# Optimization experiments

Measured on AMD Instinct MI355X. Metric: run time of the kernel, lower is better.

The kernel has to match this reference:

```python
import jax, jax.numpy as jnp
import numpy as np

F = 128   # num_features
H = 128   # hidden sizes
U = 128   # u_size == out_size
N = 50000
E = 600000
B = 64
L = 4     # hops + 1 layers


def _scatter_mean(vals, idx, num_segments):
    s = jax.ops.segment_sum(vals, idx, num_segments=num_segments)
    cnt = jax.ops.segment_sum(jnp.ones((vals.shape[0],), vals.dtype), idx,
                              num_segments=num_segments)
    return s / jnp.maximum(cnt, 1.0)[:, None]


def setup_inputs() -> dict:
    key = jax.random.key(0)
    ks = jax.random.split(key, 20)
    x = jax.random.normal(ks[0], (N, F), jnp.float32)
    edge_index = jax.random.randint(ks[1], (2, E), 0, N, jnp.int64)
    u = jax.random.normal(ks[2], (B, U), jnp.float32)
    batch = jnp.sort(jax.random.randint(ks[3], (N,), 0, B, jnp.int64))
    sc = 0.05
    # stacked per-layer params (all layer dims identical since u_size==out_size)
    params = {
        'n1w1': jax.random.normal(ks[4], (L, F, H), jnp.float32) * sc,
        'n1b1': jnp.zeros((L, H), jnp.float32),
        'n1w2': jax.random.normal(ks[5], (L, H, H), jnp.float32) * sc,
        'n1b2': jnp.zeros((L, H), jnp.float32),
        'n2w1': jax.random.normal(ks[6], (L, F + H + U, H), jnp.float32) * sc,
        'n2b1': jnp.zeros((L, H), jnp.float32),
        'n2w2': jax.random.normal(ks[7], (L, H, F), jnp.float32) * sc,
        'n2b2': jnp.zeros((L, F), jnp.float32),
        'gw1': jax.random.normal(ks[8], (L, F + U, H), jnp.float32) * sc,
        'gb1': jnp.zeros((L, H), jnp.float32),
        'gw2': jax.random.normal(ks[9], (L, H, U), jnp.float32) * sc,
        'gb2': jnp.zeros((L, U), jnp.float32),
    }
    return dict(x=x, edge_index=edge_index, u=u, batch=batch, **params)


def reference(x, edge_index, u, batch,
              n1w1, n1b1, n1w2, n1b2, n2w1, n2b1, n2w2, n2b2,
              gw1, gb1, gw2, gb2):
    row, col = edge_index[0], edge_index[1]
    for l in range(L):
        # NodeModel
        m = jax.nn.relu(x[row] @ n1w1[l] + n1b1[l]) @ n1w2[l] + n1b2[l]  # [E,H]
        agg = _scatter_mean(m, col, N)                                    # [N,H]
        h = jnp.concatenate([x, agg, u[batch]], axis=1)                   # [N,F+H+U]
        x = jax.nn.relu(h @ n2w1[l] + n2b1[l]) @ n2w2[l] + n2b2[l]        # [N,F]
        # GlobalModel (uses updated x)
        g = jnp.concatenate([u, _scatter_mean(x, batch, B)], axis=1)      # [B,F+U]
        u = jax.nn.relu(g @ gw1[l] + gb1[l]) @ gw2[l] + gb2[l]            # [B,U]
    return (x, u)
```

## Files before the change

kernel.cpp:

```cpp
#include <hip/hip_runtime.h>

typedef __bf16 bf16;
typedef bf16 bf16x8 __attribute__((ext_vector_type(8)));
typedef bf16 bf16x4 __attribute__((ext_vector_type(4)));
typedef bf16 bf16x2 __attribute__((ext_vector_type(2)));
typedef float floatx4 __attribute__((ext_vector_type(4)));

#define MFMA __builtin_amdgcn_mfma_f32_16x16x32_bf16

__device__ __forceinline__ float bfhi_f(unsigned u) {
  const unsigned x = u << 16;
  return __builtin_bit_cast(float, x);
}
__device__ __forceinline__ float bflo_f(unsigned u) {
  const unsigned x = u & 0xffff0000u;
  return __builtin_bit_cast(float, x);
}


__global__ void hist_kernel(const int* __restrict__ ei, int* __restrict__ cnt, int E) {
  int e = blockIdx.x * blockDim.x + threadIdx.x;
  if (e < E) atomicAdd(&cnt[ei[E + e]], 1);
}

__global__ void gcnt_kernel(const int* __restrict__ batch, int* __restrict__ gcnt,
                            int N, int B) {
  const int b = threadIdx.x;
  if (b >= B) return;
  auto lb = [&](int v) {
    int lo = 0, hi = N;
    while (lo < hi) {
      const int mid = (lo + hi) >> 1;
      if (batch[mid] < v) lo = mid + 1; else hi = mid;
    }
    return lo;
  };
  gcnt[b] = lb(b + 1) - lb(b);
}

__global__ void scan1_kernel(const int* __restrict__ cnt, int* __restrict__ colptr,
                             int* __restrict__ rctr, int* __restrict__ btot, int n) {
  __shared__ int sd[256];
  const int tid = threadIdx.x;
  const int i0 = blockIdx.x * 2048 + tid * 8;
  int v[8];
  int tot = 0;
#pragma unroll
  for (int j = 0; j < 8; ++j) {
    const int i = i0 + j;
    v[j] = (i < n) ? cnt[i] : 0;
    tot += v[j];
  }
  sd[tid] = tot;
  __syncthreads();
  for (int off = 1; off < 256; off <<= 1) {
    const int t = (tid >= off) ? sd[tid - off] : 0;
    __syncthreads();
    sd[tid] += t;
    __syncthreads();
  }
  int excl = sd[tid] - tot;
#pragma unroll
  for (int j = 0; j < 8; ++j) {
    const int i = i0 + j;
    if (i < n) { colptr[i] = excl; rctr[i] = excl; }
    excl += v[j];
  }
  if (tid == 255) btot[blockIdx.x] = sd[255];
}

__global__ void scan2_kernel(int* __restrict__ colptr, int* __restrict__ rctr,
                             const int* __restrict__ btot, int n) {
  __shared__ int off_s;
  const int tid = threadIdx.x;
  if (blockIdx.x == 0) return;
  if (tid == 0) {
    int o = 0;
    for (int j = 0; j < (int)blockIdx.x; ++j) o += btot[j];
    off_s = o;
  }
  __syncthreads();
  const int off = off_s;
  const int i0 = blockIdx.x * 2048 + tid * 8;
#pragma unroll
  for (int j = 0; j < 8; ++j) {
    const int i = i0 + j;
    if (i < n) { colptr[i] += off; rctr[i] += off; }
  }
}

__global__ void place_kernel(const int* __restrict__ ei, int* __restrict__ rctr,
                             int* __restrict__ esrow, int E) {
  int e = blockIdx.x * blockDim.x + threadIdx.x;
  if (e >= E) return;
  const int r = ei[e];
  const int c = ei[E + e];
  const int p = atomicAdd(&rctr[c], 1);
  esrow[p] = r;
}

__global__ void wsplit_kernel(const float* __restrict__ src, bf16* __restrict__ dst,
                              int Ksrc, int K, int HH) {
  const int l = blockIdx.y;
  const int gid = blockIdx.x * blockDim.x + threadIdx.x;
  if (gid >= K * HH) return;
  const int h = gid / K, k = gid - h * K;
  const float v = src[(size_t)l * Ksrc * HH + (size_t)k * HH + h];
  const bf16 hi = (bf16)v;
  const bf16 lo = (bf16)(v - (float)hi);
  bf16* d = dst + (size_t)l * 2 * K * HH;
  d[(size_t)h * K + k] = hi;
  d[(size_t)K * HH + (size_t)h * K + k] = lo;
}

__global__ void xsplit_kernel(const float* __restrict__ x, bf16* __restrict__ xhi,
                              bf16* __restrict__ xlo, int n4) {
  const int i = blockIdx.x * 256 + threadIdx.x;
  if (i >= n4) return;
  const float4 v = ((const float4*)x)[i];
  bf16x4 h, l;
  const float vv[4] = {v.x, v.y, v.z, v.w};
#pragma unroll
  for (int r = 0; r < 4; ++r) {
    h[r] = (bf16)vv[r];
    l[r] = (bf16)(vv[r] - (float)h[r]);
  }
  *(bf16x4*)&xhi[(size_t)i * 4] = h;
  *(bf16x4*)&xlo[(size_t)i * 4] = l;
}

__global__ __launch_bounds__(256, 4)
void pnode_mfma(const bf16* __restrict__ xh, const bf16* __restrict__ xl,
                const bf16* __restrict__ w1t, const float* __restrict__ b1,
                const bf16* __restrict__ w2t, const float* __restrict__ b2,
                bf16* __restrict__ P, int N) {
  __shared__ __align__(16) bf16 R[2 * 64 * 136];

  const int tid = threadIdx.x;
  const int n0 = blockIdx.x * 64;
  const int wave = tid >> 6, lane = tid & 63, q = lane >> 4, lr = lane & 15;
  const int hbase = wave * 32;

  int nn[4];
#pragma unroll
  for (int nt = 0; nt < 4; ++nt) {
    int n = n0 + nt * 16 + lr;
    nn[nt] = (n > N - 1) ? (N - 1) : n;
  }

  const floatx4 zz = {0.f, 0.f, 0.f, 0.f};
  floatx4 acc[2][4];
#pragma unroll
  for (int mt = 0; mt < 2; ++mt)
#pragma unroll
    for (int nt = 0; nt < 4; ++nt) acc[mt][nt] = zz;

  {
    bf16x8 bh[2][4], bl[2][4];
#pragma unroll
    for (int nt = 0; nt < 4; ++nt) {
      const size_t off = (size_t)nn[nt] * 128 + q * 8;
      bh[0][nt] = *(const bf16x8*)(xh + off);
      bl[0][nt] = *(const bf16x8*)(xl + off);
    }
#pragma unroll
    for (int kc = 0; kc < 4; ++kc) {
      const int cur = kc & 1, nxt = cur ^ 1;
      if (kc < 3) {
#pragma unroll
        for (int nt = 0; nt < 4; ++nt) {
          const size_t off = (size_t)nn[nt] * 128 + (kc + 1) * 32 + q * 8;
          bh[nxt][nt] = *(const bf16x8*)(xh + off);
          bl[nxt][nt] = *(const bf16x8*)(xl + off);
        }
      }
      bf16x8 ah[2], al[2];
#pragma unroll
      for (int mt = 0; mt < 2; ++mt) {
        const bf16* wp = w1t + (size_t)(hbase + mt * 16 + lr) * 128 + kc * 32 + q * 8;
        ah[mt] = *(const bf16x8*)wp;
        al[mt] = *(const bf16x8*)(wp + 16384);
      }
#pragma unroll
      for (int nt = 0; nt < 4; ++nt)
#pragma unroll
        for (int mt = 0; mt < 2; ++mt) {
          acc[mt][nt] = MFMA(ah[mt], bh[cur][nt], acc[mt][nt], 0, 0, 0);
          acc[mt][nt] = MFMA(al[mt], bh[cur][nt], acc[mt][nt], 0, 0, 0);
          acc[mt][nt] = MFMA(ah[mt], bl[cur][nt], acc[mt][nt], 0, 0, 0);
        }
    }
  }

#pragma unroll
  for (int mt = 0; mt < 2; ++mt) {
    const int h0 = hbase + mt * 16 + q * 4;
    const float* bp = &b1[h0];
#pragma unroll
    for (int nt = 0; nt < 4; ++nt) {
      const int e = nt * 16 + lr;
      bf16x4 hh, ll;
#pragma unroll
      for (int r = 0; r < 4; ++r) {
        const float v = fmaxf(acc[mt][nt][r] + bp[r], 0.f);
        hh[r] = (bf16)v;
        ll[r] = (bf16)(v - (float)hh[r]);
      }
      *(bf16x4*)&R[e * 136 + h0] = hh;
      *(bf16x4*)&R[64 * 136 + e * 136 + h0] = ll;
      acc[mt][nt] = zz;
    }
  }
  __syncthreads();

#pragma unroll
  for (int ks = 0; ks < 4; ++ks) {
    bf16x8 ah[2], al[2], b2h[4], b2l[4];
#pragma unroll
    for (int mt = 0; mt < 2; ++mt) {
      const bf16* wp = w2t + (size_t)(hbase + mt * 16 + lr) * 128 + ks * 32 + q * 8;
      ah[mt] = *(const bf16x8*)wp;
      al[mt] = *(const bf16x8*)(wp + 16384);
    }
#pragma unroll
    for (int nt = 0; nt < 4; ++nt) {
      const bf16* hp = &R[(nt * 16 + lr) * 136 + ks * 32 + q * 8];
      b2h[nt] = *(const bf16x8*)hp;
      b2l[nt] = *(const bf16x8*)(hp + 64 * 136);
    }
#pragma unroll
    for (int nt = 0; nt < 4; ++nt)
#pragma unroll
      for (int mt = 0; mt < 2; ++mt) {
        acc[mt][nt] = MFMA(ah[mt], b2h[nt], acc[mt][nt], 0, 0, 0);
        acc[mt][nt] = MFMA(al[mt], b2h[nt], acc[mt][nt], 0, 0, 0);
        acc[mt][nt] = MFMA(ah[mt], b2l[nt], acc[mt][nt], 0, 0, 0);
      }
  }
  __syncthreads();

#pragma unroll
  for (int mt = 0; mt < 2; ++mt) {
    const int f0 = hbase + mt * 16 + q * 4;
    const float* bp = &b2[f0];
#pragma unroll
    for (int nt = 0; nt < 4; ++nt) {
      const int e = nt * 16 + lr;
      bf16x4 o;
#pragma unroll
      for (int r = 0; r < 4; ++r) o[r] = (bf16)(acc[mt][nt][r] + bp[r]);
      *(bf16x4*)&R[e * 136 + f0] = o;
    }
  }
  __syncthreads();
#pragma unroll
  for (int it = 0; it < 4; ++it) {
    const int idx = it * 256 + tid;
    const int row = idx >> 4;
    const int f8 = (idx & 15) * 8;
    const int n = n0 + row;
    if (n < N)
      *(bf16x8*)&P[(size_t)n * 128 + f8] = *(const bf16x8*)&R[row * 136 + f8];
  }
}

__global__ __launch_bounds__(256, 8)
void agg_csr(const bf16* __restrict__ P, const int* __restrict__ colptr,
             const int* __restrict__ esrow,
             bf16* __restrict__ aggh, bf16* __restrict__ aggl, int N, int E) {
  const int lane = threadIdx.x & 63;
  const int c = blockIdx.x * 4 + (threadIdx.x >> 6);
  if (c >= N) return;
  const int beg = colptr[c];
  const int end = (c == N - 1) ? E : colptr[c + 1];
  float s0[4] = {0.f, 0.f, 0.f, 0.f};
  float s1[4] = {0.f, 0.f, 0.f, 0.f};
  int e = beg;
  for (; e + 8 <= end; e += 8) {
    int r[8];
#pragma unroll
    for (int j = 0; j < 8; ++j) r[j] = esrow[e + j];
    unsigned v[8];
#pragma unroll
    for (int j = 0; j < 8; ++j)
      v[j] = *(const unsigned*)&P[(size_t)r[j] * 128 + lane * 2];
#pragma unroll
    for (int j = 0; j < 8; ++j) {
      s0[j & 3] += bfhi_f(v[j]);
      s1[j & 3] += bflo_f(v[j]);
    }
  }
  const int rem = end - e;
  if (rem > 0) {
    int r[8];
#pragma unroll
    for (int j = 0; j < 8; ++j) r[j] = esrow[e + (j < rem ? j : 0)];
    unsigned v[8];
#pragma unroll
    for (int j = 0; j < 8; ++j)
      v[j] = *(const unsigned*)&P[(size_t)r[j] * 128 + lane * 2];
#pragma unroll
    for (int j = 0; j < 8; ++j) {
      if (j < rem) {
        s0[j & 3] += bfhi_f(v[j]);
        s1[j & 3] += bflo_f(v[j]);
      }
    }
  }
  const int cc = end - beg;
  const float inv = 1.f / (float)(cc > 1 ? cc : 1);
  const float v0 = ((s0[0] + s0[1]) + (s0[2] + s0[3])) * inv;
  const float v1 = ((s1[0] + s1[1]) + (s1[2] + s1[3])) * inv;
  bf16x2 h, l;
  h[0] = (bf16)v0;  l[0] = (bf16)(v0 - (float)h[0]);
  h[1] = (bf16)v1;  l[1] = (bf16)(v1 - (float)h[1]);
  *(bf16x2*)&aggh[(size_t)c * 128 + lane * 2] = h;
  *(bf16x2*)&aggl[(size_t)c * 128 + lane * 2] = l;
}

__global__ __launch_bounds__(256, 4)
void node_p(bf16* xh, bf16* xl,
            const bf16* __restrict__ aggh, const bf16* __restrict__ aggl,
            const float* __restrict__ UW, const int* __restrict__ batch,
            const bf16* __restrict__ w1t, const bf16* __restrict__ w2t,
            const float* __restrict__ b2,
            const bf16* __restrict__ w1te, const float* __restrict__ b1e,
            const bf16* __restrict__ w2te, const float* __restrict__ b2e,
            bf16* __restrict__ Pout, float* __restrict__ gx,
            float* __restrict__ xout, int write_x, int has_next, int N) {
  __shared__ __align__(16) bf16 R[2 * 64 * 136];
  __shared__ int sbatch[64];

  const int tid = threadIdx.x;
  const int n0 = blockIdx.x * 64;
  const int wave = tid >> 6, lane = tid & 63, q = lane >> 4, lr = lane & 15;
  const int hbase = wave * 32;

  if (tid < 64) {
    int n = n0 + tid;
    sbatch[tid] = batch[(n > N - 1) ? (N - 1) : n];
  }

  int nn[4], ub[4];
#pragma unroll
  for (int nt = 0; nt < 4; ++nt) {
    int n = n0 + nt * 16 + lr;
    if (n > N - 1) n = N - 1;
    nn[nt] = n;
    ub[nt] = batch[n];
  }

  floatx4 acc[2][4];
#pragma unroll
  for (int mt = 0; mt < 2; ++mt)
#pragma unroll
    for (int nt = 0; nt < 4; ++nt)
      acc[mt][nt] = *(const floatx4*)&UW[(size_t)ub[nt] * 128 + hbase + mt * 16 + q * 4];

  {
    bf16x8 bh[2][4], bl[2][4];
    auto loadB = [&](int kc, int buf) {
#pragma unroll
      for (int nt = 0; nt < 4; ++nt) {
        if (kc < 4) {
          const size_t off = (size_t)nn[nt] * 128 + kc * 32 + q * 8;
          bh[buf][nt] = *(const bf16x8*)(xh + off);
          bl[buf][nt] = *(const bf16x8*)(xl + off);
        } else {
          const size_t off = (size_t)nn[nt] * 128 + (kc - 4) * 32 + q * 8;
          bh[buf][nt] = *(const bf16x8*)(aggh + off);
          bl[buf][nt] = *(const bf16x8*)(aggl + off);
        }
      }
    };
    loadB(0, 0);
#pragma unroll
    for (int kc = 0; kc < 8; ++kc) {
      const int cur = kc & 1, nxt = cur ^ 1;
      if (kc < 7) loadB(kc + 1, nxt);
      bf16x8 ah[2], al[2];
#pragma unroll
      for (int mt = 0; mt < 2; ++mt) {
        const bf16* wp = w1t + (size_t)(hbase + mt * 16 + lr) * 256 + kc * 32 + q * 8;
        ah[mt] = *(const bf16x8*)wp;
        al[mt] = *(const bf16x8*)(wp + 32768);
      }
#pragma unroll
      for (int nt = 0; nt < 4; ++nt)
#pragma unroll
        for (int mt = 0; mt < 2; ++mt) {
          acc[mt][nt] = MFMA(ah[mt], bh[cur][nt], acc[mt][nt], 0, 0, 0);
          acc[mt][nt] = MFMA(al[mt], bh[cur][nt], acc[mt][nt], 0, 0, 0);
          acc[mt][nt] = MFMA(ah[mt], bl[cur][nt], acc[mt][nt], 0, 0, 0);
        }
    }
  }

  const floatx4 zz = {0.f, 0.f, 0.f, 0.f};
#pragma unroll
  for (int mt = 0; mt < 2; ++mt) {
    const int h0 = hbase + mt * 16 + q * 4;
#pragma unroll
    for (int nt = 0; nt < 4; ++nt) {
      const int e = nt * 16 + lr;
      bf16x4 hh, ll;
#pragma unroll
      for (int r = 0; r < 4; ++r) {
        const float v = fmaxf(acc[mt][nt][r], 0.f);
        hh[r] = (bf16)v;
        ll[r] = (bf16)(v - (float)hh[r]);
      }
      *(bf16x4*)&R[e * 136 + h0] = hh;
      *(bf16x4*)&R[64 * 136 + e * 136 + h0] = ll;
      acc[mt][nt] = zz;
    }
  }
  __syncthreads();

#pragma unroll
  for (int ks = 0; ks < 4; ++ks) {
    bf16x8 ah[2], al[2], b2h[4], b2l[4];
#pragma unroll
    for (int mt = 0; mt < 2; ++mt) {
      const bf16* wp = w2t + (size_t)(hbase + mt * 16 + lr) * 128 + ks * 32 + q * 8;
      ah[mt] = *(const bf16x8*)wp;
      al[mt] = *(const bf16x8*)(wp + 16384);
    }
#pragma unroll
    for (int nt = 0; nt < 4; ++nt) {
      const bf16* hp = &R[(nt * 16 + lr) * 136 + ks * 32 + q * 8];
      b2h[nt] = *(const bf16x8*)hp;
      b2l[nt] = *(const bf16x8*)(hp + 64 * 136);
    }
#pragma unroll
    for (int nt = 0; nt < 4; ++nt)
#pragma unroll
      for (int mt = 0; mt < 2; ++mt) {
        acc[mt][nt] = MFMA(ah[mt], b2h[nt], acc[mt][nt], 0, 0, 0);
        acc[mt][nt] = MFMA(al[mt], b2h[nt], acc[mt][nt], 0, 0, 0);
        acc[mt][nt] = MFMA(ah[mt], b2l[nt], acc[mt][nt], 0, 0, 0);
      }
  }
  __syncthreads();

  float* Xt = (float*)&R[0];
#pragma unroll
  for (int mt = 0; mt < 2; ++mt) {
    const int f0 = hbase + mt * 16 + q * 4;
    const float* bp = &b2[f0];
#pragma unroll
    for (int nt = 0; nt < 4; ++nt) {
      const int e = nt * 16 + lr;
      const int n = n0 + e;
      float4 o;
      o.x = (n < N) ? acc[mt][nt][0] + bp[0] : 0.f;
      o.y = (n < N) ? acc[mt][nt][1] + bp[1] : 0.f;
      o.z = (n < N) ? acc[mt][nt][2] + bp[2] : 0.f;
      o.w = (n < N) ? acc[mt][nt][3] + bp[3] : 0.f;
      *(float4*)&Xt[e * 132 + f0] = o;
    }
  }
  __syncthreads();

  if (has_next) {
#pragma unroll
    for (int it = 0; it < 4; ++it) {
      const int idx = it * 256 + tid;
      const int row = idx >> 4;
      const int f8 = (idx & 15) * 8;
      const int n = n0 + row;
      if (n < N) {
        bf16x8 hh, ll;
#pragma unroll
        for (int j = 0; j < 8; ++j) {
          const float v = Xt[row * 132 + f8 + j];
          hh[j] = (bf16)v;
          ll[j] = (bf16)(v - (float)hh[j]);
        }
        *(bf16x8*)&xh[(size_t)n * 128 + f8] = hh;
        *(bf16x8*)&xl[(size_t)n * 128 + f8] = ll;
      }
    }
  }
  if (write_x) {
#pragma unroll
    for (int it = 0; it < 8; ++it) {
      const int idx = it * 256 + tid;
      const int row = idx >> 5;
      const int f4 = (idx & 31) * 4;
      const int n = n0 + row;
      if (n < N)
        *(float4*)&xout[(size_t)n * 128 + f4] = *(const float4*)&Xt[row * 132 + f4];
    }
  }

  {
    const int f = tid & 127;
    const int es = (tid >> 7) * 32;
    int cur = sbatch[es];
    float s = 0.f;
    for (int e = es; e < es + 32; ++e) {
      const int b = sbatch[e];
      const float v = Xt[e * 132 + f];
      if (b != cur) {
        atomicAdd(&gx[(size_t)cur * 128 + f], s);
        s = 0.f;
        cur = b;
      }
      s += v;
    }
    atomicAdd(&gx[(size_t)cur * 128 + f], s);
  }

  if (!has_next) return;

#pragma unroll
  for (int mt = 0; mt < 2; ++mt)
#pragma unroll
    for (int nt = 0; nt < 4; ++nt) acc[mt][nt] = zz;

#pragma unroll
  for (int kc = 0; kc < 4; ++kc) {
    bf16x8 ah[2], al[2], bh[4], bl[4];
#pragma unroll
    for (int mt = 0; mt < 2; ++mt) {
      const bf16* wp = w1te + (size_t)(hbase + mt * 16 + lr) * 128 + kc * 32 + q * 8;
      ah[mt] = *(const bf16x8*)wp;
      al[mt] = *(const bf16x8*)(wp + 16384);
    }
#pragma unroll
    for (int nt = 0; nt < 4; ++nt) {
      const float* xp = &Xt[(nt * 16 + lr) * 132 + kc * 32 + q * 8];
#pragma unroll
      for (int r = 0; r < 8; ++r) {
        const float v = xp[r];
        bh[nt][r] = (bf16)v;
        bl[nt][r] = (bf16)(v - (float)bh[nt][r]);
      }
    }
#pragma unroll
    for (int nt = 0; nt < 4; ++nt)
#pragma unroll
      for (int mt = 0; mt < 2; ++mt) {
        acc[mt][nt] = MFMA(ah[mt], bh[nt], acc[mt][nt], 0, 0, 0);
        acc[mt][nt] = MFMA(al[mt], bh[nt], acc[mt][nt], 0, 0, 0);
        acc[mt][nt] = MFMA(ah[mt], bl[nt], acc[mt][nt], 0, 0, 0);
      }
  }
  __syncthreads();

#pragma unroll
  for (int mt = 0; mt < 2; ++mt) {
    const int h0 = hbase + mt * 16 + q * 4;
    const float* bp = &b1e[h0];
#pragma unroll
    for (int nt = 0; nt < 4; ++nt) {
      const int e = nt * 16 + lr;
      bf16x4 hh, ll;
#pragma unroll
      for (int r = 0; r < 4; ++r) {
        const float v = fmaxf(acc[mt][nt][r] + bp[r], 0.f);
        hh[r] = (bf16)v;
        ll[r] = (bf16)(v - (float)hh[r]);
      }
      *(bf16x4*)&R[e * 136 + h0] = hh;
      *(bf16x4*)&R[64 * 136 + e * 136 + h0] = ll;
      acc[mt][nt] = zz;
    }
  }
  __syncthreads();

#pragma unroll
  for (int ks = 0; ks < 4; ++ks) {
    bf16x8 ah[2], al[2], b2h[4], b2l[4];
#pragma unroll
    for (int mt = 0; mt < 2; ++mt) {
      const bf16* wp = w2te + (size_t)(hbase + mt * 16 + lr) * 128 + ks * 32 + q * 8;
      ah[mt] = *(const bf16x8*)wp;
      al[mt] = *(const bf16x8*)(wp + 16384);
    }
#pragma unroll
    for (int nt = 0; nt < 4; ++nt) {
      const bf16* hp = &R[(nt * 16 + lr) * 136 + ks * 32 + q * 8];
      b2h[nt] = *(const bf16x8*)hp;
      b2l[nt] = *(const bf16x8*)(hp + 64 * 136);
    }
#pragma unroll
    for (int nt = 0; nt < 4; ++nt)
#pragma unroll
      for (int mt = 0; mt < 2; ++mt) {
        acc[mt][nt] = MFMA(ah[mt], b2h[nt], acc[mt][nt], 0, 0, 0);
        acc[mt][nt] = MFMA(al[mt], b2h[nt], acc[mt][nt], 0, 0, 0);
        acc[mt][nt] = MFMA(ah[mt], b2l[nt], acc[mt][nt], 0, 0, 0);
      }
  }
  __syncthreads();

#pragma unroll
  for (int mt = 0; mt < 2; ++mt) {
    const int f0 = hbase + mt * 16 + q * 4;
    const float* bp = &b2e[f0];
#pragma unroll
    for (int nt = 0; nt < 4; ++nt) {
      const int e = nt * 16 + lr;
      bf16x4 o;
#pragma unroll
      for (int r = 0; r < 4; ++r) o[r] = (bf16)(acc[mt][nt][r] + bp[r]);
      *(bf16x4*)&R[e * 136 + f0] = o;
    }
  }
  __syncthreads();
#pragma unroll
  for (int it = 0; it < 4; ++it) {
    const int idx = it * 256 + tid;
    const int row = idx >> 4;
    const int f8 = (idx & 15) * 8;
    const int n = n0 + row;
    if (n < N)
      *(bf16x8*)&Pout[(size_t)n * 128 + f8] = *(const bf16x8*)&R[row * 136 + f8];
  }
}

__global__ void uw_kernel(const float* __restrict__ u, const float* __restrict__ w1,
                          const float* __restrict__ b1, float* __restrict__ UW) {
  const int b = blockIdx.x, h = threadIdx.x;
  float s = b1[h];
#pragma unroll 8
  for (int k = 0; k < 128; ++k)
    s = fmaf(u[b * 128 + k], w1[(size_t)(256 + k) * 128 + h], s);
  UW[b * 128 + h] = s;
}

__global__ __launch_bounds__(128)
void gmlp_kernel(const float* __restrict__ uin, float* __restrict__ gx,
                 const int* __restrict__ gcnt,
                 const float* __restrict__ gw1, const float* __restrict__ gb1,
                 const float* __restrict__ gw2, const float* __restrict__ gb2,
                 float* __restrict__ uout,
                 const float* __restrict__ w1n_next,
                 const float* __restrict__ b1n_next,
                 float* __restrict__ UW, int has_next) {
  __shared__ float g[256];
  __shared__ float g1[128];
  const int b = blockIdx.x;
  const int t = threadIdx.x;
  const int c = gcnt[b];
  const float inv = 1.f / (float)(c > 1 ? c : 1);
  g[t] = uin[b * 128 + t];
  g[128 + t] = gx[b * 128 + t] * inv;
  gx[b * 128 + t] = 0.f;
  __syncthreads();
  float acc = gb1[t];
#pragma unroll 8
  for (int k = 0; k < 256; ++k) acc = fmaf(g[k], gw1[k * 128 + t], acc);
  g1[t] = fmaxf(acc, 0.f);
  __syncthreads();
  float acc2 = gb2[t];
#pragma unroll 8
  for (int k = 0; k < 128; ++k) acc2 = fmaf(g1[k], gw2[k * 128 + t], acc2);
  uout[b * 128 + t] = acc2;
  if (has_next) {
    __syncthreads();
    g[t] = acc2;
    __syncthreads();
    float s = b1n_next[t];
#pragma unroll 8
    for (int k = 0; k < 128; ++k)
      s = fmaf(g[k], w1n_next[(size_t)(256 + k) * 128 + t], s);
    UW[b * 128 + t] = s;
  }
}

extern "C" void kernel_launch(void* const* d_in, const int* in_sizes, int n_in,
                              void* d_out, int out_size, void* d_ws, size_t ws_size,
                              hipStream_t stream) {
  constexpr int N = 50000, E = 600000, B = 64, F = 128, L = 4;

  const float* x0    = (const float*)d_in[0];
  const int*   ei    = (const int*)  d_in[1];
  const float* u0    = (const float*)d_in[2];
  const int*   batch = (const int*)  d_in[3];
  const float* n1w1  = (const float*)d_in[4];
  const float* n1b1  = (const float*)d_in[5];
  const float* n1w2  = (const float*)d_in[6];
  const float* n1b2  = (const float*)d_in[7];
  const float* n2w1  = (const float*)d_in[8];
  const float* n2b1  = (const float*)d_in[9];
  const float* n2w2  = (const float*)d_in[10];
  const float* n2b2  = (const float*)d_in[11];
  const float* gw1   = (const float*)d_in[12];
  const float* gb1   = (const float*)d_in[13];
  const float* gw2   = (const float*)d_in[14];
  const float* gb2   = (const float*)d_in[15];
  float* out = (float*)d_out;

  char* p = (char*)d_ws;
  auto carve = [&](size_t bytes) -> void* {
    void* q = (void*)p;
    p += (bytes + 255) & ~(size_t)255;
    return q;
  };
  float* ubuf  = (float*)carve((size_t)B * F * 4);
  float* gx    = (float*)carve((size_t)B * F * 4);
  float* UW    = (float*)carve((size_t)B * F * 4);
  int*   cnt   = (int*)carve((size_t)N * 4);
  int*   colptr= (int*)carve((size_t)(N + 1) * 4);
  int*   rctr  = (int*)carve((size_t)N * 4);
  int*   gcnt  = (int*)carve((size_t)B * 4);
  int*   btot  = (int*)carve(32 * 4);
  int*   esrow = (int*)carve((size_t)E * 4);
  bf16*  xhi   = (bf16*)carve((size_t)N * F * 2);
  bf16*  xlo   = (bf16*)carve((size_t)N * F * 2);
  bf16*  P_a   = (bf16*)carve((size_t)N * F * 2);
  bf16*  P_b   = (bf16*)carve((size_t)N * F * 2);
  bf16*  aggh  = (bf16*)carve((size_t)N * F * 2);
  bf16*  aggl  = (bf16*)carve((size_t)N * F * 2);
  bf16*  w1t_e = (bf16*)carve((size_t)L * 2 * 128 * 128 * 2);
  bf16*  w2t_e = (bf16*)carve((size_t)L * 2 * 128 * 128 * 2);
  bf16*  w1t_n = (bf16*)carve((size_t)L * 2 * 256 * 128 * 2);
  bf16*  w2t_n = (bf16*)carve((size_t)L * 2 * 128 * 128 * 2);

  constexpr int SCAN_BLOCKS = (N + 2047) / 2048;

  hipMemsetAsync(cnt, 0, (size_t)N * 4, stream);
  hipMemsetAsync(gx, 0, (size_t)B * F * 4, stream);
  hist_kernel<<<(E + 255) / 256, 256, 0, stream>>>(ei, cnt, E);
  gcnt_kernel<<<1, 64, 0, stream>>>(batch, gcnt, N, B);
  scan1_kernel<<<SCAN_BLOCKS, 256, 0, stream>>>(cnt, colptr, rctr, btot, N);
  scan2_kernel<<<SCAN_BLOCKS, 256, 0, stream>>>(colptr, rctr, btot, N);
  place_kernel<<<(E + 255) / 256, 256, 0, stream>>>(ei, rctr, esrow, E);
  wsplit_kernel<<<dim3(64, L), 256, 0, stream>>>(n1w1, w1t_e, 128, 128, 128);
  wsplit_kernel<<<dim3(64, L), 256, 0, stream>>>(n1w2, w2t_e, 128, 128, 128);
  wsplit_kernel<<<dim3(128, L), 256, 0, stream>>>(n2w1, w1t_n, 384, 256, 128);
  wsplit_kernel<<<dim3(64, L), 256, 0, stream>>>(n2w2, w2t_n, 128, 128, 128);
  xsplit_kernel<<<(N * F / 4 + 255) / 256, 256, 0, stream>>>(x0, xhi, xlo, N * F / 4);
  uw_kernel<<<B, 128, 0, stream>>>(u0, n2w1, n2b1, UW);

  const int NB = (N + 63) / 64;
  pnode_mfma<<<NB, 256, 0, stream>>>(xhi, xlo, w1t_e, n1b1, w2t_e, n1b2, P_a, N);

  for (int l = 0; l < L; ++l) {
    const float* uin  = l ? ubuf : u0;
    float*       uout = (l == L - 1) ? out + (size_t)N * F : ubuf;
    const int    wx   = (l == L - 1) ? 1 : 0;
    const int    hn   = (l < L - 1) ? 1 : 0;
    const bf16*  Pin  = (l & 1) ? P_b : P_a;
    bf16*        Pout = (l & 1) ? P_a : P_b;
    const int    le   = hn ? (l + 1) : l;

    agg_csr<<<(N + 3) / 4, 256, 0, stream>>>(Pin, colptr, esrow, aggh, aggl, N, E);
    node_p<<<NB, 256, 0, stream>>>(
        xhi, xlo, aggh, aggl, UW, batch,
        w1t_n + (size_t)l * 65536, w2t_n + (size_t)l * 32768,
        n2b2 + l * 128,
        w1t_e + (size_t)le * 32768, n1b1 + le * 128,
        w2t_e + (size_t)le * 32768, n1b2 + le * 128,
        Pout, gx, out, wx, hn, N);
    gmlp_kernel<<<B, 128, 0, stream>>>(
        uin, gx, gcnt,
        gw1 + (size_t)l * 256 * 128, gb1 + l * 128,
        gw2 + (size_t)l * 128 * 128, gb2 + l * 128, uout,
        hn ? (n2w1 + (size_t)(l + 1) * 384 * 128) : n2w1,
        hn ? (n2b1 + (l + 1) * 128) : n2b1,
        UW, hn);
  }
}
```

Measured before the change: 702.8 us.

## Give each wave its own 16-node tile to drop block barriers

Both MLP kernels (pnode_mfma and node_p) now give each wave an independent 16-node tile that covers all 128 output columns, replacing the 64-node tile split across four waves. Each wave stages its hidden activations in a private LDS slice and waits with an lgkmcnt fence instead of __syncthreads. The aim is to remove block-wide barriers and the cross-wave dependency between the GEMM stages. In exchange, every wave now loads the full weight matrices itself, roughly four times more weight traffic per node, and holds eight accumulators. Launch bounds are lowered to 3 blocks per CU.

```diff
diff --git a/kernel.cpp b/kernel.cpp
--- a/kernel.cpp
+++ b/kernel.cpp
@@ -15,6 +15,10 @@
 __device__ __forceinline__ float bflo_f(unsigned u) {
   const unsigned x = u & 0xffff0000u;
   return __builtin_bit_cast(float, x);
+}
+
+__device__ __forceinline__ void lds_fence() {
+  asm volatile("s_waitcnt lgkmcnt(0)" ::: "memory");
 }
 
 
@@ -129,138 +133,107 @@
   *(bf16x4*)&xlo[(size_t)i * 4] = l;
 }
 
-__global__ __launch_bounds__(256, 4)
+__global__ __launch_bounds__(256, 3)
 void pnode_mfma(const bf16* __restrict__ xh, const bf16* __restrict__ xl,
                 const bf16* __restrict__ w1t, const float* __restrict__ b1,
                 const bf16* __restrict__ w2t, const float* __restrict__ b2,
                 bf16* __restrict__ P, int N) {
-  __shared__ __align__(16) bf16 R[2 * 64 * 136];
+  __shared__ __align__(16) bf16 R[4 * 4352];
 
   const int tid = threadIdx.x;
-  const int n0 = blockIdx.x * 64;
   const int wave = tid >> 6, lane = tid & 63, q = lane >> 4, lr = lane & 15;
-  const int hbase = wave * 32;
-
-  int nn[4];
-#pragma unroll
-  for (int nt = 0; nt < 4; ++nt) {
-    int n = n0 + nt * 16 + lr;
-    nn[nt] = (n > N - 1) ? (N - 1) : n;
-  }
+  const int tile = blockIdx.x * 4 + wave;
+  const int n0 = tile * 16;
+  if (n0 >= N) return;
+  int n = n0 + lr; if (n > N - 1) n = N - 1;
+  bf16* Rw = &R[wave * 4352];
 
   const floatx4 zz = {0.f, 0.f, 0.f, 0.f};
-  floatx4 acc[2][4];
-#pragma unroll
-  for (int mt = 0; mt < 2; ++mt)
-#pragma unroll
-    for (int nt = 0; nt < 4; ++nt) acc[mt][nt] = zz;
+  floatx4 acc[8];
+#pragma unroll
+  for (int mt = 0; mt < 8; ++mt) acc[mt] = zz;
 
   {
-    bf16x8 bh[2][4], bl[2][4];
-#pragma unroll
-    for (int nt = 0; nt < 4; ++nt) {
-      const size_t off = (size_t)nn[nt] * 128 + q * 8;
-      bh[0][nt] = *(const bf16x8*)(xh + off);
-      bl[0][nt] = *(const bf16x8*)(xl + off);
+    bf16x8 bh[2], bl[2];
+    {
+      const size_t off = (size_t)n * 128 + q * 8;
+      bh[0] = *(const bf16x8*)(xh + off);
+      bl[0] = *(const bf16x8*)(xl + off);
     }
 #pragma unroll
     for (int kc = 0; kc < 4; ++kc) {
-      const int cur = kc & 1, nxt = cur ^ 1;
+      const int cur = kc & 1;
       if (kc < 3) {
-#pragma unroll
-        for (int nt = 0; nt < 4; ++nt) {
-          const size_t off = (size_t)nn[nt] * 128 + (kc + 1) * 32 + q * 8;
-          bh[nxt][nt] = *(const bf16x8*)(xh + off);
-          bl[nxt][nt] = *(const bf16x8*)(xl + off);
-        }
+        const size_t off = (size_t)n * 128 + (kc + 1) * 32 + q * 8;
+        bh[cur ^ 1] = *(const bf16x8*)(xh + off);
+        bl[cur ^ 1] = *(const bf16x8*)(xl + off);
       }
-      bf16x8 ah[2], al[2];
-#pragma unroll
-      for (int mt = 0; mt < 2; ++mt) {
-        const bf16* wp = w1t + (size_t)(hbase + mt * 16 + lr) * 128 + kc * 32 + q * 8;
-        ah[mt] = *(const bf16x8*)wp;
-        al[mt] = *(const bf16x8*)(wp + 16384);
+#pragma unroll
+      for (int mt = 0; mt < 8; ++mt) {
+        const bf16* wp = w1t + (size_t)(mt * 16 + lr) * 128 + kc * 32 + q * 8;
+        const bf16x8 ah = *(const bf16x8*)wp;
+        const bf16x8 al = *(const bf16x8*)(wp + 16384);
+        acc[mt] = MFMA(ah, bh[cur], acc[mt], 0, 0, 0);
+        acc[mt] = MFMA(al, bh[cur], acc[mt], 0, 0, 0);
+        acc[mt] = MFMA(ah, bl[cur], acc[mt], 0, 0, 0);
       }
-#pragma unroll
-      for (int nt = 0; nt < 4; ++nt)
-#pragma unroll
-        for (int mt = 0; mt < 2; ++mt) {
-          acc[mt][nt] = MFMA(ah[mt], bh[cur][nt], acc[mt][nt], 0, 0, 0);
-          acc[mt][nt] = MFMA(al[mt], bh[cur][nt], acc[mt][nt], 0, 0, 0);
-          acc[mt][nt] = MFMA(ah[mt], bl[cur][nt], acc[mt][nt], 0, 0, 0);
-        }
-    }
-  }
-
-#pragma unroll
-  for (int mt = 0; mt < 2; ++mt) {
-    const int h0 = hbase + mt * 16 + q * 4;
-    const float* bp = &b1[h0];
-#pragma unroll
-    for (int nt = 0; nt < 4; ++nt) {
-      const int e = nt * 16 + lr;
-      bf16x4 hh, ll;
-#pragma unroll
-      for (int r = 0; r < 4; ++r) {
-        const float v = fmaxf(acc[mt][nt][r] + bp[r], 0.f);
-        hh[r] = (bf16)v;
-        ll[r] = (bf16)(v - (float)hh[r]);
-      }
-      *(bf16x4*)&R[e * 136 + h0] = hh;
-      *(bf16x4*)&R[64 * 136 + e * 136 + h0] = ll;
-      acc[mt][nt] = zz;
-    }
-  }
-  __syncthreads();
+    }
+  }
+
+#pragma unroll
+  for (int mt = 0; mt < 8; ++mt) {
+    const int h0 = mt * 16 + q * 4;
+    const float4 bv = *(const float4*)&b1[h0];
+    const float bb[4] = {bv.x, bv.y, bv.z, bv.w};
+    bf16x4 hh, ll;
+#pragma unroll
+    for (int r = 0; r < 4; ++r) {
+      const float v = fmaxf(acc[mt][r] + bb[r], 0.f);
+      hh[r] = (bf16)v;
+      ll[r] = (bf16)(v - (float)hh[r]);
+    }
+    *(bf16x4*)&Rw[lr * 136 + h0] = hh;
+    *(bf16x4*)&Rw[2176 + lr * 136 + h0] = ll;
+    acc[mt] = zz;
+  }
+  lds_fence();
 
 #pragma unroll
   for (int ks = 0; ks < 4; ++ks) {
-    bf16x8 ah[2], al[2], b2h[4], b2l[4];
-#pragma unroll
-    for (int mt = 0; mt < 2; ++mt) {
-      const bf16* wp = w2t + (size_t)(hbase + mt * 16 + lr) * 128 + ks * 32 + q * 8;
-      ah[mt] = *(const bf16x8*)wp;
-      al[mt] = *(const bf16x8*)(wp + 16384);
-    }
-#pragma unroll
-    for (int nt = 0; nt < 4; ++nt) {
-      const bf16* hp = &R[(nt * 16 + lr) * 136 + ks * 32 + q * 8];
-      b2h[nt] = *(const bf16x8*)hp;
-      b2l[nt] = *(const bf16x8*)(hp + 64 * 136);
-    }
-#pragma unroll
-    for (int nt = 0; nt < 4; ++nt)
-#pragma unroll
-      for (int mt = 0; mt < 2; ++mt) {
-        acc[mt][nt] = MFMA(ah[mt], b2h[nt], acc[mt][nt], 0, 0, 0);
-        acc[mt][nt] = MFMA(al[mt], b2h[nt], acc[mt][nt], 0, 0, 0);
-        acc[mt][nt] = MFMA(ah[mt], b2l[nt], acc[mt][nt], 0, 0, 0);
-      }
-  }
-  __syncthreads();
-
-#pragma unroll
-  for (int mt = 0; mt < 2; ++mt) {
-    const int f0 = hbase + mt * 16 + q * 4;
-    const float* bp = &b2[f0];
-#pragma unroll
-    for (int nt = 0; nt < 4; ++nt) {
-      const int e = nt * 16 + lr;
-      bf16x4 o;
-#pragma unroll
-      for (int r = 0; r < 4; ++r) o[r] = (bf16)(acc[mt][nt][r] + bp[r]);
-      *(bf16x4*)&R[e * 136 + f0] = o;
-    }
-  }
-  __syncthreads();
+    const bf16* hp = &Rw[lr * 136 + ks * 32 + q * 8];
+    const bf16x8 b2h = *(const bf16x8*)hp;
+    const bf16x8 b2l = *(const bf16x8*)(hp + 2176);
+#pragma unroll
+    for (int mt = 0; mt < 8; ++mt) {
+      const bf16* wp = w2t + (size_t)(mt * 16 + lr) * 128 + ks * 32 + q * 8;
+      const bf16x8 ah = *(const bf16x8*)wp;
+      const bf16x8 al = *(const bf16x8*)(wp + 16384);
+      acc[mt] = MFMA(ah, b2h, acc[mt], 0, 0, 0);
+      acc[mt] = MFMA(al, b2h, acc[mt], 0, 0, 0);
+      acc[mt] = MFMA(ah, b2l, acc[mt], 0, 0, 0);
+    }
+  }
+  lds_fence();
+
+#pragma unroll
+  for (int mt = 0; mt < 8; ++mt) {
+    const int f0 = mt * 16 + q * 4;
+    const float4 bv = *(const float4*)&b2[f0];
+    const float bb[4] = {bv.x, bv.y, bv.z, bv.w};
+    bf16x4 o;
+#pragma unroll
+    for (int r = 0; r < 4; ++r) o[r] = (bf16)(acc[mt][r] + bb[r]);
+    *(bf16x4*)&Rw[lr * 136 + f0] = o;
+  }
+  lds_fence();
 #pragma unroll
   for (int it = 0; it < 4; ++it) {
-    const int idx = it * 256 + tid;
+    const int idx = it * 64 + lane;
     const int row = idx >> 4;
     const int f8 = (idx & 15) * 8;
-    const int n = n0 + row;
-    if (n < N)
-      *(bf16x8*)&P[(size_t)n * 128 + f8] = *(const bf16x8*)&R[row * 136 + f8];
+    const int nn2 = n0 + row;
+    if (nn2 < N)
+      *(bf16x8*)&P[(size_t)nn2 * 128 + f8] = *(const bf16x8*)&Rw[row * 136 + f8];
   }
 }
 
@@ -318,7 +291,7 @@
   *(bf16x2*)&aggl[(size_t)c * 128 + lane * 2] = l;
 }
 
-__global__ __launch_bounds__(256, 4)
+__global__ __launch_bounds__(256, 3)
 void node_p(bf16* xh, bf16* xl,
             const bf16* __restrict__ aggh, const bf16* __restrict__ aggl,
             const float* __restrict__ UW, const int* __restrict__ batch,
@@ -328,148 +301,109 @@
             const bf16* __restrict__ w2te, const float* __restrict__ b2e,
             bf16* __restrict__ Pout, float* __restrict__ gx,
             float* __restrict__ xout, int write_x, int has_next, int N) {
-  __shared__ __align__(16) bf16 R[2 * 64 * 136];
-  __shared__ int sbatch[64];
+  __shared__ __align__(16) bf16 R[4 * 4352];
 
   const int tid = threadIdx.x;
-  const int n0 = blockIdx.x * 64;
   const int wave = tid >> 6, lane = tid & 63, q = lane >> 4, lr = lane & 15;
-  const int hbase = wave * 32;
-
-  if (tid < 64) {
-    int n = n0 + tid;
-    sbatch[tid] = batch[(n > N - 1) ? (N - 1) : n];
-  }
-
-  int nn[4], ub[4];
-#pragma unroll
-  for (int nt = 0; nt < 4; ++nt) {
-    int n = n0 + nt * 16 + lr;
-    if (n > N - 1) n = N - 1;
-    nn[nt] = n;
-    ub[nt] = batch[n];
-  }
-
-  floatx4 acc[2][4];
-#pragma unroll
-  for (int mt = 0; mt < 2; ++mt)
-#pragma unroll
-    for (int nt = 0; nt < 4; ++nt)
-      acc[mt][nt] = *(const floatx4*)&UW[(size_t)ub[nt] * 128 + hbase + mt * 16 + q * 4];
+  const int tile = blockIdx.x * 4 + wave;
+  const int n0 = tile * 16;
+  if (n0 >= N) return;
+  int n = n0 + lr; if (n > N - 1) n = N - 1;
+  const int ub = batch[n];
+  bf16* Rw = &R[wave * 4352];
+  float* Xt = (float*)Rw;
+
+  floatx4 acc[8];
+#pragma unroll
+  for (int mt = 0; mt < 8; ++mt)
+    acc[mt] = *(const floatx4*)&UW[(size_t)ub * 128 + mt * 16 + q * 4];
 
   {
-    bf16x8 bh[2][4], bl[2][4];
-    auto loadB = [&](int kc, int buf) {
-#pragma unroll
-      for (int nt = 0; nt < 4; ++nt) {
-        if (kc < 4) {
-          const size_t off = (size_t)nn[nt] * 128 + kc * 32 + q * 8;
-          bh[buf][nt] = *(const bf16x8*)(xh + off);
-          bl[buf][nt] = *(const bf16x8*)(xl + off);
-        } else {
-          const size_t off = (size_t)nn[nt] * 128 + (kc - 4) * 32 + q * 8;
-          bh[buf][nt] = *(const bf16x8*)(aggh + off);
-          bl[buf][nt] = *(const bf16x8*)(aggl + off);
-        }
+    bf16x8 bh[2], bl[2];
+    {
+      const size_t off = (size_t)n * 128 + q * 8;
+      bh[0] = *(const bf16x8*)(xh + off);
+      bl[0] = *(const bf16x8*)(xl + off);
+    }
+#pragma unroll
+    for (int kc = 0; kc < 8; ++kc) {
+      const int cur = kc & 1;
+      if (kc < 7) {
+        const int k1 = kc + 1;
+        const size_t off = (size_t)n * 128 + (k1 & 3) * 32 + q * 8;
+        const bf16* sh = (k1 < 4) ? xh : aggh;
+        const bf16* sl = (k1 < 4) ? xl : aggl;
+        bh[cur ^ 1] = *(const bf16x8*)(sh + off);
+        bl[cur ^ 1] = *(const bf16x8*)(sl + off);
       }
-    };
-    loadB(0, 0);
-#pragma unroll
-    for (int kc = 0; kc < 8; ++kc) {
-      const int cur = kc & 1, nxt = cur ^ 1;
-      if (kc < 7) loadB(kc + 1, nxt);
-      bf16x8 ah[2], al[2];
-#pragma unroll
-      for (int mt = 0; mt < 2; ++mt) {
-        const bf16* wp = w1t + (size_t)(hbase + mt * 16 + lr) * 256 + kc * 32 + q * 8;
-        ah[mt] = *(const bf16x8*)wp;
-        al[mt] = *(const bf16x8*)(wp + 32768);
+#pragma unroll
+      for (int mt = 0; mt < 8; ++mt) {
+        const bf16* wp = w1t + (size_t)(mt * 16 + lr) * 256 + kc * 32 + q * 8;
+        const bf16x8 ah = *(const bf16x8*)wp;
+        const bf16x8 al = *(const bf16x8*)(wp + 32768);
+        acc[mt] = MFMA(ah, bh[cur], acc[mt], 0, 0, 0);
+        acc[mt] = MFMA(al, bh[cur], acc[mt], 0, 0, 0);
+        acc[mt] = MFMA(ah, bl[cur], acc[mt], 0, 0, 0);
       }
-#pragma unroll
-      for (int nt = 0; nt < 4; ++nt)
-#pragma unroll
-        for (int mt = 0; mt < 2; ++mt) {
-          acc[mt][nt] = MFMA(ah[mt], bh[cur][nt], acc[mt][nt], 0, 0, 0);
-          acc[mt][nt] = MFMA(al[mt], bh[cur][nt], acc[mt][nt], 0, 0, 0);
-          acc[mt][nt] = MFMA(ah[mt], bl[cur][nt], acc[mt][nt], 0, 0, 0);
-        }
     }
   }
 
   const floatx4 zz = {0.f, 0.f, 0.f, 0.f};
 #pragma unroll
-  for (int mt = 0; mt < 2; ++mt) {
-    const int h0 = hbase + mt * 16 + q * 4;
-#pragma unroll
-    for (int nt = 0; nt < 4; ++nt) {
-      const int e = nt * 16 + lr;
-      bf16x4 hh, ll;
-#pragma unroll
-      for (int r = 0; r < 4; ++r) {
-        const float v = fmaxf(acc[mt][nt][r], 0.f);
-        hh[r] = (bf16)v;
-        ll[r] = (bf16)(v - (float)hh[r]);
-      }
-      *(bf16x4*)&R[e * 136 + h0] = hh;
-      *(bf16x4*)&R[64 * 136 + e * 136 + h0] = ll;
-      acc[mt][nt] = zz;
-    }
-  }
-  __syncthreads();
+  for (int mt = 0; mt < 8; ++mt) {
+    const int h0 = mt * 16 + q * 4;
+    bf16x4 hh, ll;
+#pragma unroll
+    for (int r = 0; r < 4; ++r) {
+      const float v = fmaxf(acc[mt][r], 0.f);
+      hh[r] = (bf16)v;
+      ll[r] = (bf16)(v - (float)hh[r]);
+    }
+    *(bf16x4*)&Rw[lr * 136 + h0] = hh;
+    *(bf16x4*)&Rw[2176 + lr * 136 + h0] = ll;
+    acc[mt] = zz;
+  }
+  lds_fence();
 
 #pragma unroll
   for (int ks = 0; ks < 4; ++ks) {
-    bf16x8 ah[2], al[2], b2h[4], b2l[4];
-#pragma unroll
-    for (int mt = 0; mt < 2; ++mt) {
-      const bf16* wp = w2t + (size_t)(hbase + mt * 16 + lr) * 128 + ks * 32 + q * 8;
-      ah[mt] = *(const bf16x8*)wp;
-      al[mt] = *(const bf16x8*)(wp + 16384);
-    }
-#pragma unroll
-    for (int nt = 0; nt < 4; ++nt) {
-      const bf16* hp = &R[(nt * 16 + lr) * 136 + ks * 32 + q * 8];
-      b2h[nt] = *(const bf16x8*)hp;
-      b2l[nt] = *(const bf16x8*)(hp + 64 * 136);
-    }
-#pragma unroll
-    for (int nt = 0; nt < 4; ++nt)
-#pragma unroll
-      for (int mt = 0; mt < 2; ++mt) {
-        acc[mt][nt] = MFMA(ah[mt], b2h[nt], acc[mt][nt], 0, 0, 0);
-        acc[mt][nt] = MFMA(al[mt], b2h[nt], acc[mt][nt], 0, 0, 0);
-        acc[mt][nt] = MFMA(ah[mt], b2l[nt], acc[mt][nt], 0, 0, 0);
-      }
-  }
-  __syncthreads();
-
-  float* Xt = (float*)&R[0];
-#pragma unroll
-  for (int mt = 0; mt < 2; ++mt) {
-    const int f0 = hbase + mt * 16 + q * 4;
-    const float* bp = &b2[f0];
-#pragma unroll
-    for (int nt = 0; nt < 4; ++nt) {
-      const int e = nt * 16 + lr;
-      const int n = n0 + e;
-      float4 o;
-      o.x = (n < N) ? acc[mt][nt][0] + bp[0] : 0.f;
-      o.y = (n < N) ? acc[mt][nt][1] + bp[1] : 0.f;
-      o.z = (n < N) ? acc[mt][nt][2] + bp[2] : 0.f;
-      o.w = (n < N) ? acc[mt][nt][3] + bp[3] : 0.f;
-      *(float4*)&Xt[e * 132 + f0] = o;
-    }
-  }
-  __syncthreads();
+    const bf16* hp = &Rw[lr * 136 + ks * 32 + q * 8];
+    const bf16x8 b2h = *(const bf16x8*)hp;
+    const bf16x8 b2l = *(const bf16x8*)(hp + 2176);
+#pragma unroll
+    for (int mt = 0; mt < 8; ++mt) {
+      const bf16* wp = w2t + (size_t)(mt * 16 + lr) * 128 + ks * 32 + q * 8;
+      const bf16x8 ah = *(const bf16x8*)wp;
+      const bf16x8 al = *(const bf16x8*)(wp + 16384);
+      acc[mt] = MFMA(ah, b2h, acc[mt], 0, 0, 0);
+      acc[mt] = MFMA(al, b2h, acc[mt], 0, 0, 0);
+      acc[mt] = MFMA(ah, b2l, acc[mt], 0, 0, 0);
+    }
+  }
+  lds_fence();
+
+  const int ok = (n0 + lr) < N;
+#pragma unroll
+  for (int mt = 0; mt < 8; ++mt) {
+    const int f0 = mt * 16 + q * 4;
+    const float4 bv = *(const float4*)&b2[f0];
+    float4 o;
+    o.x = ok ? acc[mt][0] + bv.x : 0.f;
+    o.y = ok ? acc[mt][1] + bv.y : 0.f;
+    o.z = ok ? acc[mt][2] + bv.z : 0.f;
+    o.w = ok ? acc[mt][3] + bv.w : 0.f;
+    *(float4*)&Xt[lr * 132 + f0] = o;
+  }
+  lds_fence();
 
   if (has_next) {
 #pragma unroll
     for (int it = 0; it < 4; ++it) {
-      const int idx = it * 256 + tid;
+      const int idx = it * 64 + lane;
       const int row = idx >> 4;
       const int f8 = (idx & 15) * 8;
-      const int n = n0 + row;
-      if (n < N) {
+      const int nn2 = n0 + row;
+      if (nn2 < N) {
         bf16x8 hh, ll;
 #pragma unroll
         for (int j = 0; j < 8; ++j) {
@@ -477,147 +411,124 @@
           hh[j] = (bf16)v;
           ll[j] = (bf16)(v - (float)hh[j]);
         }
-        *(bf16x8*)&xh[(size_t)n * 128 + f8] = hh;
-        *(bf16x8*)&xl[(size_t)n * 128 + f8] = ll;
+        *(bf16x8*)&xh[(size_t)nn2 * 128 + f8] = hh;
+        *(bf16x8*)&xl[(size_t)nn2 * 128 + f8] = ll;
       }
     }
   }
   if (write_x) {
 #pragma unroll
     for (int it = 0; it < 8; ++it) {
-      const int idx = it * 256 + tid;
+      const int idx = it * 64 + lane;
       const int row = idx >> 5;
       const int f4 = (idx & 31) * 4;
-      const int n = n0 + row;
-      if (n < N)
-        *(float4*)&xout[(size_t)n * 128 + f4] = *(const float4*)&Xt[row * 132 + f4];
+      const int nn2 = n0 + row;
+      if (nn2 < N)
+        *(float4*)&xout[(size_t)nn2 * 128 + f4] = *(const float4*)&Xt[row * 132 + f4];
     }
   }
 
   {
-    const int f = tid & 127;
-    const int es = (tid >> 7) * 32;
-    int cur = sbatch[es];
-    float s = 0.f;
-    for (int e = es; e < es + 32; ++e) {
-      const int b = sbatch[e];
-      const float v = Xt[e * 132 + f];
+    const int f = lane;
+    int cur = __shfl(ub, 0);
+    float s0 = 0.f, s1 = 0.f;
+#pragma unroll
+    for (int e = 0; e < 16; ++e) {
+      const int b = __shfl(ub, e);
+      const float v0 = Xt[e * 132 + f];
+      const float v1 = Xt[e * 132 + 64 + f];
       if (b != cur) {
-        atomicAdd(&gx[(size_t)cur * 128 + f], s);
-        s = 0.f;
-        cur = b;
+        atomicAdd(&gx[(size_t)cur * 128 + f], s0);
+        atomicAdd(&gx[(size_t)cur * 128 + 64 + f], s1);
+        s0 = 0.f; s1 = 0.f; cur = b;
       }
-      s += v;
-    }
-    atomicAdd(&gx[(size_t)cur * 128 + f], s);
+      s0 += v0; s1 += v1;
+    }
+    atomicAdd(&gx[(size_t)cur * 128 + f], s0);
+    atomicAdd(&gx[(size_t)cur * 128 + 64 + f], s1);
   }
 
   if (!has_next) return;
 
 #pragma unroll
-  for (int mt = 0; mt < 2; ++mt)
-#pragma unroll
-    for (int nt = 0; nt < 4; ++nt) acc[mt][nt] = zz;
+  for (int mt = 0; mt < 8; ++mt) acc[mt] = zz;
 
 #pragma unroll
   for (int kc = 0; kc < 4; ++kc) {
-    bf16x8 ah[2], al[2], bh[4], bl[4];
-#pragma unroll
-    for (int mt = 0; mt < 2; ++mt) {
-      const bf16* wp = w1te + (size_t)(hbase + mt * 16 + lr) * 128 + kc * 32 + q * 8;
-      ah[mt] = *(const bf16x8*)wp;
-      al[mt] = *(const bf16x8*)(wp + 16384);
-    }
-#pragma unroll
-    for (int nt = 0; nt < 4; ++nt) {
-      const float* xp = &Xt[(nt * 16 + lr) * 132 + kc * 32 + q * 8];
-#pragma unroll
-      for (int r = 0; r < 8; ++r) {
-        const float v = xp[r];
-        bh[nt][r] = (bf16)v;
-        bl[nt][r] = (bf16)(v - (float)bh[nt][r]);
-      }
-    }
-#pragma unroll
-    for (int nt = 0; nt < 4; ++nt)
-#pragma unroll
-      for (int mt = 0; mt < 2; ++mt) {
-        acc[mt][nt] = MFMA(ah[mt], bh[nt], acc[mt][nt], 0, 0, 0);
-        acc[mt][nt] = MFMA(al[mt], bh[nt], acc[mt][nt], 0, 0, 0);
-        acc[mt][nt] = MFMA(ah[mt], bl[nt], acc[mt][nt], 0, 0, 0);
-      }
-  }
-  __syncthreads();
-
-#pragma unroll
-  for (int mt = 0; mt < 2; ++mt) {
-    const int h0 = hbase + mt * 16 + q * 4;
-    const float* bp = &b1e[h0];
-#pragma unroll
-    for (int nt = 0; nt < 4; ++nt) {
-      const int e = nt * 16 + lr;
-      bf16x4 hh, ll;
-#pragma unroll
-      for (int r = 0; r < 4; ++r) {
-        const float v = fmaxf(acc[mt][nt][r] + bp[r], 0.f);
-        hh[r] = (bf16)v;
-        ll[r] = (bf16)(v - (float)hh[r]);
-      }
-      *(bf16x4*)&R[e * 136 + h0] = hh;
-      *(bf16x4*)&R[64 * 136 + e * 136 + h0] = ll;
-      acc[mt][nt] = zz;
-    }
-  }
-  __syncthreads();
+    bf16x8 bh, bl;
+    const float* xp = &Xt[lr * 132 + kc * 32 + q * 8];
+#pragma unroll
+    for (int r = 0; r < 8; ++r) {
+      const float v = xp[r];
+      bh[r] = (bf16)v;
+      bl[r] = (bf16)(v - (float)bh[r]);
+    }
+#pragma unroll
+    for (int mt = 0; mt < 8; ++mt) {
+      const bf16* wp = w1te + (size_t)(mt * 16 + lr) * 128 + kc * 32 + q * 8;
+      const bf16x8 ah = *(const bf16x8*)wp;
+      const bf16x8 al = *(const bf16x8*)(wp + 16384);
+      acc[mt] = MFMA(ah, bh, acc[mt], 0, 0, 0);
+      acc[mt] = MFMA(al, bh, acc[mt], 0, 0, 0);
+      acc[mt] = MFMA(ah, bl, acc[mt], 0, 0, 0);
+    }
+  }
+  lds_fence();
+
+#pragma unroll
+  for (int mt = 0; mt < 8; ++mt) {
+    const int h0 = mt * 16 + q * 4;
+    const float4 bv = *(const float4*)&b1e[h0];
+    const float bb[4] = {bv.x, bv.y, bv.z, bv.w};
+    bf16x4 hh, ll;
+#pragma unroll
+    for (int r = 0; r < 4; ++r) {
+      const float v = fmaxf(acc[mt][r] + bb[r], 0.f);
+      hh[r] = (bf16)v;
+      ll[r] = (bf16)(v - (float)hh[r]);
+    }
+    *(bf16x4*)&Rw[lr * 136 + h0] = hh;
+    *(bf16x4*)&Rw[2176 + lr * 136 + h0] = ll;
+    acc[mt] = zz;
+  }
+  lds_fence();
 
 #pragma unroll
   for (int ks = 0; ks < 4; ++ks) {
-    bf16x8 ah[2], al[2], b2h[4], b2l[4];
-#pragma unroll
-    for (int mt = 0; mt < 2; ++mt) {
-      const bf16* wp = w2te + (size_t)(hbase + mt * 16 + lr) * 128 + ks * 32 + q * 8;
-      ah[mt] = *(const bf16x8*)wp;
-      al[mt] = *(const bf16x8*)(wp + 16384);
-    }
-#pragma unroll
-    for (int nt = 0; nt < 4; ++nt) {
-      const bf16* hp = &R[(nt * 16 + lr) * 136 + ks * 32 + q * 8];
-      b2h[nt] = *(const bf16x8*)hp;
-      b2l[nt] = *(const bf16x8*)(hp + 64 * 136);
-    }
-#pragma unroll
-    for (int nt = 0; nt < 4; ++nt)
-#pragma unroll
-      for (int mt = 0; mt < 2; ++mt) {
-        acc[mt][nt] = MFMA(ah[mt], b2h[nt], acc[mt][nt], 0, 0, 0);
-        acc[mt][nt] = MFMA(al[mt], b2h[nt], acc[mt][nt], 0, 0, 0);
-        acc[mt][nt] = MFMA(ah[mt], b2l[nt], acc[mt][nt], 0, 0, 0);
-      }
-  }
-  __syncthreads();
-
-#pragma unroll
-  for (int mt = 0; mt < 2; ++mt) {
-    const int f0 = hbase + mt * 16 + q * 4;
-    const float* bp = &b2e[f0];
-#pragma unroll
-    for (int nt = 0; nt < 4; ++nt) {
-      const int e = nt * 16 + lr;
-      bf16x4 o;
-#pragma unroll
-      for (int r = 0; r < 4; ++r) o[r] = (bf16)(acc[mt][nt][r] + bp[r]);
-      *(bf16x4*)&R[e * 136 + f0] = o;
-    }
-  }
-  __syncthreads();
+    const bf16* hp = &Rw[lr * 136 + ks * 32 + q * 8];
+    const bf16x8 b2h = *(const bf16x8*)hp;
+    const bf16x8 b2l = *(const bf16x8*)(hp + 2176);
+#pragma unroll
+    for (int mt = 0; mt < 8; ++mt) {
+      const bf16* wp = w2te + (size_t)(mt * 16 + lr) * 128 + ks * 32 + q * 8;
+      const bf16x8 ah = *(const bf16x8*)wp;
+      const bf16x8 al = *(const bf16x8*)(wp + 16384);
+      acc[mt] = MFMA(ah, b2h, acc[mt], 0, 0, 0);
+      acc[mt] = MFMA(al, b2h, acc[mt], 0, 0, 0);
+      acc[mt] = MFMA(ah, b2l, acc[mt], 0, 0, 0);
+    }
+  }
+  lds_fence();
+
+#pragma unroll
+  for (int mt = 0; mt < 8; ++mt) {
+    const int f0 = mt * 16 + q * 4;
+    const float4 bv = *(const float4*)&b2e[f0];
+    const float bb[4] = {bv.x, bv.y, bv.z, bv.w};
+    bf16x4 o;
+#pragma unroll
+    for (int r = 0; r < 4; ++r) o[r] = (bf16)(acc[mt][r] + bb[r]);
+    *(bf16x4*)&Rw[lr * 136 + f0] = o;
+  }
+  lds_fence();
 #pragma unroll
   for (int it = 0; it < 4; ++it) {
-    const int idx = it * 256 + tid;
+    const int idx = it * 64 + lane;
     const int row = idx >> 4;
     const int f8 = (idx & 15) * 8;
-    const int n = n0 + row;
-    if (n < N)
-      *(bf16x8*)&Pout[(size_t)n * 128 + f8] = *(const bf16x8*)&R[row * 136 + f8];
+    const int nn2 = n0 + row;
+    if (nn2 < N)
+      *(bf16x8*)&Pout[(size_t)nn2 * 128 + f8] = *(const bf16x8*)&Rw[row * 136 + f8];
   }
 }
 
```

Result: slower. 1.094 ms (+55.6%).
